# Performance work log

Hardware: AMD Instinct MI355X
Metric: run time of the kernel (lower is better)

Reference implementation:

```python
import jax, jax.numpy as jnp
import numpy as np

TOPK = 13
NUM_CLASSES = 80
ALPHA = 1.0
BETA = 6.0
EPS = 1e-9


def _ciou(gt, pd, eps=1e-7):
    """CIoU between gt (B,M,1,4) and pd (B,1,N,4) xyxy boxes -> (B,M,N)."""
    g_x1, g_y1, g_x2, g_y2 = (gt[..., i] for i in range(4))
    p_x1, p_y1, p_x2, p_y2 = (pd[..., i] for i in range(4))
    iw = jnp.clip(jnp.minimum(g_x2, p_x2) - jnp.maximum(g_x1, p_x1), 0.0)
    ih = jnp.clip(jnp.minimum(g_y2, p_y2) - jnp.maximum(g_y1, p_y1), 0.0)
    inter = iw * ih
    w1, h1 = g_x2 - g_x1, g_y2 - g_y1 + eps
    w2, h2 = p_x2 - p_x1, p_y2 - p_y1 + eps
    union = w1 * h1 + w2 * h2 - inter + eps
    iou = inter / union
    cw = jnp.maximum(g_x2, p_x2) - jnp.minimum(g_x1, p_x1)  # enclosing box
    ch = jnp.maximum(g_y2, p_y2) - jnp.minimum(g_y1, p_y1)
    c2 = cw * cw + ch * ch + eps
    rho2 = ((p_x1 + p_x2 - g_x1 - g_x2) ** 2 + (p_y1 + p_y2 - g_y1 - g_y2) ** 2) / 4.0
    v = (4.0 / jnp.pi ** 2) * (jnp.arctan(w2 / h2) - jnp.arctan(w1 / h1)) ** 2
    a = jax.lax.stop_gradient(v / (v - iou + (1.0 + eps)))  # torch.no_grad alpha
    return iou - (rho2 / c2 + v * a)


def setup_inputs() -> dict:
    key = jax.random.key(0)
    ks = jax.random.split(key, 7)
    B, N, M, C = 16, 8400, 32, NUM_CLASSES
    pd_scores = jax.random.uniform(ks[0], (B, N, C), dtype=jnp.float32)
    # YOLO-style anchor centers for 640x640, strides 8/16/32 -> 8400 points
    pts = []
    for s in (8, 16, 32):
        g = 640 // s
        xs = (jnp.arange(g, dtype=jnp.float32) + 0.5) * s
        xx, yy = jnp.meshgrid(xs, xs, indexing="xy")
        pts.append(jnp.stack([xx.ravel(), yy.ravel()], axis=-1))
    anc_points = jnp.concatenate(pts, axis=0)  # (8400, 2)
    ctr = anc_points[None] + jax.random.normal(ks[1], (B, N, 2)) * 8.0
    wh = jax.random.uniform(ks[2], (B, N, 2), minval=8.0, maxval=128.0)
    pd_bboxes = jnp.concatenate([ctr - wh / 2, ctr + wh / 2], axis=-1)
    gctr = jax.random.uniform(ks[3], (B, M, 2), minval=32.0, maxval=608.0)
    gwh = jax.random.uniform(ks[4], (B, M, 2), minval=16.0, maxval=256.0)
    gt_bboxes = jnp.concatenate([gctr - gwh / 2, gctr + gwh / 2], axis=-1)
    gt_labels = jax.random.randint(ks[5], (B, M, 1), 0, C)
    counts = jax.random.randint(ks[6], (B, 1), 1, M + 1)
    mask_gt = (jnp.arange(M)[None, :] < counts)[..., None]  # (B, M, 1) bool prefix-valid
    return {"pd_scores": pd_scores, "pd_bboxes": pd_bboxes, "anc_points": anc_points,
            "gt_labels": gt_labels, "gt_bboxes": gt_bboxes, "mask_gt": mask_gt}


def reference(pd_scores, pd_bboxes, anc_points, gt_labels, gt_bboxes, mask_gt):
    B, N, C = pd_scores.shape
    M = gt_bboxes.shape[1]
    mask_gt2 = mask_gt[..., 0]  # (B, M) bool
    # --- anchors whose centers lie inside each GT box ---
    lt = gt_bboxes[:, :, None, :2]  # (B, M, 1, 2)
    rb = gt_bboxes[:, :, None, 2:]
    anc = anc_points[None, None]    # (1, 1, N, 2)
    deltas = jnp.concatenate([anc - lt, rb - anc], axis=-1)  # (B, M, N, 4)
    mask_in_gts = jnp.min(deltas, axis=-1) > 1e-9            # (B, M, N)
    valid = mask_in_gts & mask_gt2[:, :, None]
    # --- alignment metric = score^alpha * ciou^beta (masked) ---
    cls = gt_labels[..., 0]                      # (B, M)
    scores_t = jnp.swapaxes(pd_scores, 1, 2)     # (B, C, N)
    bbox_scores = jnp.where(valid, scores_t[jnp.arange(B)[:, None], cls], 0.0)  # (B, M, N)
    overlaps = jnp.where(valid, jnp.clip(_ciou(gt_bboxes[:, :, None], pd_bboxes[:, None]), 0.0), 0.0)
    align_metric = bbox_scores ** ALPHA * overlaps ** BETA
    # --- top-k candidate anchors per GT ---
    _, topk_idx = jax.lax.top_k(align_metric, TOPK)          # (B, M, TOPK)
    bi = jnp.arange(B)[:, None, None]
    mi = jnp.arange(M)[None, :, None]
    src = jnp.broadcast_to(mask_gt2[:, :, None], topk_idx.shape)
    mask_topk = jnp.zeros((B, M, N), dtype=bool).at[bi, mi, topk_idx].set(src)
    mask_pos = mask_topk & valid                             # (B, M, N)
    # --- resolve anchors claimed by multiple GTs: keep highest CIoU ---
    fg_count = jnp.sum(mask_pos, axis=1)                     # (B, N)
    best_gt = jnp.argmax(overlaps, axis=1)                   # (B, N)
    is_max = jnp.arange(M)[None, :, None] == best_gt[:, None, :]
    mask_pos_f = jnp.where(fg_count[:, None, :] > 1, is_max, mask_pos).astype(pd_scores.dtype)
    fg_mask = jnp.sum(mask_pos_f, axis=1)                    # (B, N) float 0/1
    target_gt_idx = jnp.argmax(mask_pos_f, axis=1)           # (B, N)
    # --- gather targets ---
    brow = jnp.arange(B)[:, None]
    target_labels = cls[brow, target_gt_idx]                 # (B, N)
    target_bboxes = gt_bboxes[brow, target_gt_idx]           # (B, N, 4)
    target_scores = jax.nn.one_hot(target_labels, C, dtype=jnp.float32) * fg_mask[..., None]
    # --- normalize scores by per-GT best metric/overlap ---
    align_metric = align_metric * mask_pos_f
    pos_align = jnp.max(align_metric, axis=-1, keepdims=True)            # (B, M, 1)
    pos_over = jnp.max(overlaps * mask_pos_f, axis=-1, keepdims=True)    # (B, M, 1)
    norm_align = jnp.max(align_metric * pos_over / (pos_align + EPS), axis=1)  # (B, N)
    target_scores = target_scores * norm_align[..., None]
    return target_labels, target_bboxes, target_scores, fg_mask > 0, target_gt_idx
```

## Files before the change

### kernel.cpp

```cpp
#include <hip/hip_runtime.h>
#include <math.h>

#define B_ 16
#define N_ 8400
#define M_ 32
#define C_ 80
#define TOPK_ 13
#define KL_ 16

__device__ __forceinline__ bool in_gt(double ax, double ay,
    double gx1, double gy1, double gx2, double gy2) {
  return (ax - gx1 > 1e-9) && (ay - gy1 > 1e-9) &&
         (gx2 - ax > 1e-9) && (gy2 - ay > 1e-9);
}

__device__ __forceinline__ double ciou_ov(
    double px1, double py1, double px2, double py2,
    double gx1, double gy1, double gx2, double gy2,
    double atp, double atg) {
  double iw = fmin(gx2, px2) - fmax(gx1, px1); iw = iw > 0.0 ? iw : 0.0;
  double ih = fmin(gy2, py2) - fmax(gy1, py1); ih = ih > 0.0 ? ih : 0.0;
  double inter = iw * ih;
  double w1 = gx2 - gx1, h1 = gy2 - gy1 + 1e-7;
  double w2 = px2 - px1, h2 = py2 - py1 + 1e-7;
  double uni = w1 * h1 + w2 * h2 - inter + 1e-7;
  double iou = inter / uni;
  double cw = fmax(gx2, px2) - fmin(gx1, px1);
  double ch = fmax(gy2, py2) - fmin(gy1, py1);
  double c2 = cw * cw + ch * ch + 1e-7;
  double dx = px1 + px2 - gx1 - gx2, dy = py1 + py2 - gy1 - gy2;
  double rho2 = (dx * dx + dy * dy) * 0.25;
  double dv = atp - atg;
  double v = (4.0 / (M_PI * M_PI)) * dv * dv;
  double a = v / (v - iou + (1.0 + 1e-7));
  double c = iou - (rho2 / c2 + v * a);
  return c > 0.0 ? c : 0.0;
}

#define MERGE_LISTS(av, ai, bv, bi)                                          \
  {                                                                          \
    _Pragma("unroll")                                                        \
    for (int j = 0; j < KL_; ++j) {                                          \
      double vb = bv[KL_ - 1 - j]; int ib = bi[KL_ - 1 - j];                 \
      bool take = (vb > av[j]) || (vb == av[j] && ib < ai[j]);               \
      av[j] = take ? vb : av[j];                                             \
      ai[j] = take ? ib : ai[j];                                             \
    }                                                                        \
    _Pragma("unroll")                                                        \
    for (int dd = 8; dd >= 1; dd >>= 1) {                                    \
      _Pragma("unroll")                                                      \
      for (int j = 0; j < KL_; ++j) {                                        \
        if (!(j & dd)) {                                                     \
          int kk = j | dd;                                                   \
          bool sw = (av[kk] > av[j]) ||                                      \
                    (av[kk] == av[j] && ai[kk] < ai[j]);                     \
          double xv = av[j]; int xi = ai[j];                                 \
          av[j] = sw ? av[kk] : av[j]; ai[j] = sw ? ai[kk] : ai[j];          \
          av[kk] = sw ? xv : av[kk];   ai[kk] = sw ? xi : ai[kk];            \
        }                                                                    \
      }                                                                      \
    }                                                                        \
  }

__global__ __launch_bounds__(256) void k_prep(
    const float* __restrict__ pd_bboxes, const float* __restrict__ gt_bboxes,
    const unsigned char* __restrict__ raw,
    double* __restrict__ atp, double* __restrict__ atg,
    unsigned char* __restrict__ mask) {
  int gid = blockIdx.x * 256 + threadIdx.x;
  if (gid < B_ * N_) {
    double x1 = pd_bboxes[(size_t)gid * 4 + 0], y1 = pd_bboxes[(size_t)gid * 4 + 1];
    double x2 = pd_bboxes[(size_t)gid * 4 + 2], y2 = pd_bboxes[(size_t)gid * 4 + 3];
    atp[gid] = atan((x2 - x1) / (y2 - y1 + 1e-7));
  }
  if (gid < B_ * M_) {
    double x1 = gt_bboxes[gid * 4 + 0], y1 = gt_bboxes[gid * 4 + 1];
    double x2 = gt_bboxes[gid * 4 + 2], y2 = gt_bboxes[gid * 4 + 3];
    atg[gid] = atan((x2 - x1) / (y2 - y1 + 1e-7));
  }
  if (blockIdx.x == 0) {
    __shared__ int s_bad;
    int t = threadIdx.x;
    if (t == 0) s_bad = 0;
    __syncthreads();
    if (t < B_) {
      int cnt = 0; bool seen0 = false; bool bad = false;
      for (int m = 0; m < M_; ++m) {
        unsigned char v = raw[t * M_ + m];
        if (v > 1) { bad = true; break; }
        if (v) { if (seen0) { bad = true; break; } ++cnt; }
        else seen0 = true;
      }
      if (cnt < 1) bad = true;
      if (bad) atomicOr(&s_bad, 1);
    }
    __syncthreads();
    bool ok = (s_bad == 0);
    const int* ri = (const int*)raw;
    for (int i = t; i < B_ * M_; i += 256)
      mask[i] = ok ? (raw[i] ? 1 : 0) : ((ri[i] != 0) ? 1 : 0);
  }
}

__global__ __launch_bounds__(256) void k_topk(
    const float* __restrict__ pd_scores, const float* __restrict__ pd_bboxes,
    const float* __restrict__ anc, const int* __restrict__ gt_labels,
    const float* __restrict__ gt_bboxes, const unsigned char* __restrict__ mask,
    const double* __restrict__ atp, const double* __restrict__ atg,
    unsigned int* __restrict__ MPB) {
  int row = blockIdx.x;
  if (!mask[row]) return;
  int b = row >> 5, m = row & 31;
  int t = threadIdx.x;

  double gx1 = gt_bboxes[row * 4 + 0], gy1 = gt_bboxes[row * 4 + 1];
  double gx2 = gt_bboxes[row * 4 + 2], gy2 = gt_bboxes[row * 4 + 3];
  double atgm = atg[row];
  int cls = gt_labels[row];

  const float4* pb4 = (const float4*)(pd_bboxes + (size_t)b * N_ * 4);
  const float2* an2 = (const float2*)anc;
  const double* ap  = atp + (size_t)b * N_;
  const float*  scp = pd_scores + (size_t)b * N_ * C_ + cls;

  double tv[KL_]; int ti[KL_];
#pragma unroll
  for (int j = 0; j < KL_; ++j) { tv[j] = -1.0; ti[j] = 0x7fffffff; }

  auto body = [&](int n) {
    float2 a2 = an2[n];
    bool val = in_gt((double)a2.x, (double)a2.y, gx1, gy1, gx2, gy2);
    double am = 0.0;
    if (val) {
      float4 pbox = pb4[n];
      double ov = ciou_ov((double)pbox.x, (double)pbox.y, (double)pbox.z,
                          (double)pbox.w, gx1, gy1, gx2, gy2, ap[n], atgm);
      double o2 = ov * ov;
      am = (double)scp[(size_t)n * C_] * (o2 * o2 * o2);
    }
    if (am > tv[TOPK_ - 1]) {
      double cv = am; int ci = n;
#pragma unroll
      for (int j = 0; j < TOPK_; ++j) {
        bool sw = (cv > tv[j]) || (cv == tv[j] && ci < ti[j]);
        double xv = tv[j]; int xi = ti[j];
        if (sw) { tv[j] = cv; ti[j] = ci; cv = xv; ci = xi; }
      }
    }
  };

  for (int it = 0; it < 32; ++it) body(t + it * 256);
  if (t < N_ - 8192) body(t + 8192);

#pragma unroll
  for (int d = 1; d <= 32; d <<= 1) {
    double bv[KL_]; int bi[KL_];
#pragma unroll
    for (int j = 0; j < KL_; ++j) {
      bv[j] = __shfl_xor(tv[j], d, 64);
      bi[j] = __shfl_xor(ti[j], d, 64);
    }
    MERGE_LISTS(tv, ti, bv, bi)
  }

  __shared__ double s_v[4 * KL_];
  __shared__ int    s_i[4 * KL_];
  __shared__ int    s_sel[TOPK_];
  int wave = t >> 6, lane = t & 63;
  if (lane == 0) {
#pragma unroll
    for (int j = 0; j < KL_; ++j) { s_v[wave * KL_ + j] = tv[j]; s_i[wave * KL_ + j] = ti[j]; }
  }
  __syncthreads();
  if (t == 0) {
    double av[KL_]; int ai[KL_];
#pragma unroll
    for (int j = 0; j < KL_; ++j) { av[j] = s_v[j]; ai[j] = s_i[j]; }
    for (int w = 1; w < 4; ++w) {
      double bv[KL_]; int bi[KL_];
#pragma unroll
      for (int j = 0; j < KL_; ++j) { bv[j] = s_v[w * KL_ + j]; bi[j] = s_i[w * KL_ + j]; }
      MERGE_LISTS(av, ai, bv, bi)
    }
#pragma unroll
    for (int j = 0; j < TOPK_; ++j) s_sel[j] = ai[j];
  }
  __syncthreads();

  if (t < TOPK_) {
    int n = s_sel[t];
    float2 a2 = an2[n];
    if (in_gt((double)a2.x, (double)a2.y, gx1, gy1, gx2, gy2))
      atomicOr(&MPB[(size_t)b * N_ + n], 1u << m);
  }
}

__global__ __launch_bounds__(256) void k_colassign(
    const float* __restrict__ pd_scores, const float* __restrict__ pd_bboxes,
    const float* __restrict__ anc, const int* __restrict__ gt_labels,
    const float* __restrict__ gt_bboxes, const unsigned char* __restrict__ mask,
    const double* __restrict__ atp, const double* __restrict__ atg,
    const unsigned int* __restrict__ MPB,
    unsigned char* __restrict__ TG, unsigned char* __restrict__ FG,
    float* __restrict__ AMC,
    unsigned int* __restrict__ PAL, unsigned int* __restrict__ POV) {
  int b = blockIdx.y;
  int n = blockIdx.x * 256 + threadIdx.x;

  __shared__ float s_g[M_][4];
  __shared__ double s_atg[M_];
  __shared__ int s_cls[M_];
  __shared__ unsigned char s_msk[M_];
  if (threadIdx.x < M_) {
    int gi = b * M_ + threadIdx.x;
    s_g[threadIdx.x][0] = gt_bboxes[gi * 4 + 0];
    s_g[threadIdx.x][1] = gt_bboxes[gi * 4 + 1];
    s_g[threadIdx.x][2] = gt_bboxes[gi * 4 + 2];
    s_g[threadIdx.x][3] = gt_bboxes[gi * 4 + 3];
    s_atg[threadIdx.x] = atg[gi];
    s_cls[threadIdx.x] = gt_labels[gi];
    s_msk[threadIdx.x] = mask[gi];
  }
  __syncthreads();
  if (n >= N_) return;

  size_t i = (size_t)b * N_ + n;
  unsigned int mpb = MPB[i];
  int cnt = __popc(mpb);
  int tg = 0; unsigned char fg = 0;
  double ov = 0.0;

  if (cnt >= 1) {
    fg = 1;
    float2 a2 = ((const float2*)anc)[n];
    float4 pbox = ((const float4*)(pd_bboxes + (size_t)b * N_ * 4))[n];
    double atpn = atp[i];
    if (cnt == 1) {
      tg = __ffs(mpb) - 1;
      double g0 = s_g[tg][0], g1 = s_g[tg][1], g2 = s_g[tg][2], g3 = s_g[tg][3];
      bool val = s_msk[tg] && in_gt((double)a2.x, (double)a2.y, g0, g1, g2, g3);
      ov = val ? ciou_ov((double)pbox.x, (double)pbox.y, (double)pbox.z,
                         (double)pbox.w, g0, g1, g2, g3, atpn, s_atg[tg]) : 0.0;
    } else {
      double best = -1.0;
      for (int mm = 0; mm < M_; ++mm) {
        double g0 = s_g[mm][0], g1 = s_g[mm][1], g2 = s_g[mm][2], g3 = s_g[mm][3];
        bool val = s_msk[mm] && in_gt((double)a2.x, (double)a2.y, g0, g1, g2, g3);
        double o = val ? ciou_ov((double)pbox.x, (double)pbox.y, (double)pbox.z,
                                 (double)pbox.w, g0, g1, g2, g3, atpn, s_atg[mm])
                       : 0.0;
        if (o > best) { best = o; tg = mm; }
      }
      ov = best;
    }
  }

  TG[i] = (unsigned char)tg;
  FG[i] = fg;

  if (fg) {
    double o2 = ov * ov;
    double am = (double)pd_scores[i * C_ + s_cls[tg]] * (o2 * o2 * o2);
    float ovf = (float)ov, amf = (float)am;
    AMC[i] = amf;
    atomicMax(&PAL[b * M_ + tg], __float_as_uint(amf));
    atomicMax(&POV[b * M_ + tg], __float_as_uint(ovf));
  }
}

__global__ __launch_bounds__(256) void k_emit(
    const int* __restrict__ gt_labels, const float* __restrict__ gt_bboxes,
    const unsigned char* __restrict__ TG, const unsigned char* __restrict__ FG,
    const float* __restrict__ AMC,
    const unsigned int* __restrict__ PAL, const unsigned int* __restrict__ POV,
    float* __restrict__ out) {
  int b = blockIdx.y;
  int n0 = blockIdx.x * 64;
  int t = threadIdx.x;

  __shared__ float s_g[M_][4];
  __shared__ int s_cls[M_];
  __shared__ float s_pal[M_], s_pov[M_];
  __shared__ float s_na[64];
  __shared__ int   s_lab[64];
  __shared__ int   s_tg[64];
  __shared__ unsigned char s_fg[64];
  if (t < M_) {
    int gi = b * M_ + t;
    s_g[t][0] = gt_bboxes[gi * 4 + 0];
    s_g[t][1] = gt_bboxes[gi * 4 + 1];
    s_g[t][2] = gt_bboxes[gi * 4 + 2];
    s_g[t][3] = gt_bboxes[gi * 4 + 3];
    s_cls[t] = gt_labels[gi];
    s_pal[t] = __uint_as_float(PAL[gi]);
    s_pov[t] = __uint_as_float(POV[gi]);
  }
  __syncthreads();

  if (t < 64) {
    int n = n0 + t;
    if (n < N_) {
      size_t i = (size_t)b * N_ + n;
      int tg = TG[i];
      unsigned char fg = FG[i];
      float na = 0.0f;
      if (fg) {
        double am = (double)AMC[i];
        na = (float)(am * (double)s_pov[tg] / ((double)s_pal[tg] + 1e-9));
      }
      s_na[t] = na; s_lab[t] = s_cls[tg]; s_tg[t] = tg; s_fg[t] = fg;
    }
  }
  __syncthreads();

  float* o0 = out;
  float* o1 = out + (size_t)B_ * N_;
  float* o2 = out + (size_t)B_ * N_ * 5;
  float* o3 = out + (size_t)B_ * N_ * 85;
  float* o4 = out + (size_t)B_ * N_ * 86;

  if (t < 64) {
    int n = n0 + t;
    if (n < N_) {
      size_t i = (size_t)b * N_ + n;
      o0[i] = (float)s_lab[t];
      o3[i] = s_fg[t] ? 1.0f : 0.0f;
      o4[i] = (float)s_tg[t];
      int tg = s_tg[t];
      ((float4*)o1)[i] = make_float4(s_g[tg][0], s_g[tg][1], s_g[tg][2], s_g[tg][3]);
    }
  }

#pragma unroll
  for (int k = 0; k < 5; ++k) {
    int id = t + k * 256;
    int a = id / 20, j = id % 20;
    int n = n0 + a;
    if (n < N_) {
      int lab = s_lab[a];
      float na = s_fg[a] ? s_na[a] : 0.0f;
      int c0 = 4 * j;
      float4 w;
      w.x = (c0 + 0 == lab) ? na : 0.0f;
      w.y = (c0 + 1 == lab) ? na : 0.0f;
      w.z = (c0 + 2 == lab) ? na : 0.0f;
      w.w = (c0 + 3 == lab) ? na : 0.0f;
      ((float4*)(o2 + ((size_t)b * N_ + n) * C_))[j] = w;
    }
  }
}

extern "C" void kernel_launch(void* const* d_in, const int* in_sizes, int n_in,
                              void* d_out, int out_size, void* d_ws, size_t ws_size,
                              hipStream_t stream) {
  const float* pd_scores = (const float*)d_in[0];
  const float* pd_bboxes = (const float*)d_in[1];
  const float* anc       = (const float*)d_in[2];
  const int*   gt_labels = (const int*)d_in[3];
  const float* gt_bboxes = (const float*)d_in[4];
  const unsigned char* mask_raw = (const unsigned char*)d_in[5];

  char* ws = (char*)d_ws;
  size_t off = 0;
  double* ATP = (double*)(ws + off); off += (size_t)B_ * N_ * 8;
  double* ATG = (double*)(ws + off); off += (size_t)B_ * M_ * 8;
  unsigned int* MPB = (unsigned int*)(ws + off); size_t z0 = off; off += (size_t)B_ * N_ * 4;
  unsigned int* PAL = (unsigned int*)(ws + off); off += (size_t)B_ * M_ * 4;
  unsigned int* POV = (unsigned int*)(ws + off); off += (size_t)B_ * M_ * 4;
  size_t zlen = off - z0;
  unsigned char* TG   = (unsigned char*)(ws + off); off += (size_t)B_ * N_;
  unsigned char* FG   = (unsigned char*)(ws + off); off += (size_t)B_ * N_;
  float* AMC = (float*)(ws + off); off += (size_t)B_ * N_ * 4;
  unsigned char* MASK = (unsigned char*)(ws + off); off += (size_t)B_ * M_;

  hipMemsetAsync(ws + z0, 0, zlen, stream);

  k_prep<<<(B_ * N_ + 255) / 256, 256, 0, stream>>>(pd_bboxes, gt_bboxes,
                                                    mask_raw, ATP, ATG, MASK);
  k_topk<<<B_ * M_, 256, 0, stream>>>(pd_scores, pd_bboxes, anc, gt_labels,
                                      gt_bboxes, MASK, ATP, ATG, MPB);
  dim3 gbn((N_ + 255) / 256, B_);
  k_colassign<<<gbn, 256, 0, stream>>>(pd_scores, pd_bboxes, anc, gt_labels,
                                       gt_bboxes, MASK, ATP, ATG, MPB,
                                       TG, FG, AMC, PAL, POV);
  dim3 gem((N_ + 63) / 64, B_);
  k_emit<<<gem, 256, 0, stream>>>(gt_labels, gt_bboxes, TG, FG, AMC, PAL, POV,
                                  (float*)d_out);
}
```

Before: 176.1 us.

## Pre-gather per-GT class scores into a contiguous buffer before top-k

Adds a kernel that streams pd_scores coalesced through shared memory and writes, for each (batch, gt) row, the score of that GT's class at every anchor into a contiguous SG buffer. k_topk and k_colassign then read SG with unit stride instead of doing strided 320-byte-apart loads from pd_scores. This trades one full coalesced pass over pd_scores (~43MB) plus a 17MB write for removing uncoalesced gathers, and adds a kernel launch and extra workspace.

```diff
diff --git a/kernel.cpp b/kernel.cpp
--- a/kernel.cpp
+++ b/kernel.cpp
@@ -7,6 +7,7 @@
 #define C_ 80
 #define TOPK_ 13
 #define KL_ 16
+#define GT_ 128
 
 __device__ __forceinline__ bool in_gt(double ax, double ay,
     double gx1, double gy1, double gx2, double gy2) {
@@ -102,9 +103,41 @@
   }
 }
 
+__global__ __launch_bounds__(256) void k_gath(
+    const float* __restrict__ pd_scores, const int* __restrict__ gt_labels,
+    float* __restrict__ SG) {
+  int b = blockIdx.y;
+  int n0 = blockIdx.x * GT_;
+  int t = threadIdx.x;
+  int nn = min(GT_, N_ - n0);
+
+  __shared__ float s_sc[GT_ * C_];
+  __shared__ int s_cls[M_];
+  if (t < M_) s_cls[t] = gt_labels[b * M_ + t];
+
+  const float4* src = (const float4*)(pd_scores + ((size_t)b * N_ + n0) * C_);
+  float4* dst = (float4*)s_sc;
+  int tot4 = nn * (C_ / 4);
+#pragma unroll
+  for (int k = 0; k < GT_ * (C_ / 4) / 256; ++k) {
+    int id = t + k * 256;
+    if (id < tot4) dst[id] = src[id];
+  }
+  __syncthreads();
+
+  int nl = t & (GT_ - 1);
+  int mh = t >> 7;
+#pragma unroll
+  for (int mm = 0; mm < M_ / 2; ++mm) {
+    int m = mm * 2 + mh;
+    if (nl < nn)
+      SG[(size_t)(b * M_ + m) * N_ + n0 + nl] = s_sc[nl * C_ + s_cls[m]];
+  }
+}
+
 __global__ __launch_bounds__(256) void k_topk(
-    const float* __restrict__ pd_scores, const float* __restrict__ pd_bboxes,
-    const float* __restrict__ anc, const int* __restrict__ gt_labels,
+    const float* __restrict__ SG, const float* __restrict__ pd_bboxes,
+    const float* __restrict__ anc,
     const float* __restrict__ gt_bboxes, const unsigned char* __restrict__ mask,
     const double* __restrict__ atp, const double* __restrict__ atg,
     unsigned int* __restrict__ MPB) {
@@ -116,12 +149,11 @@
   double gx1 = gt_bboxes[row * 4 + 0], gy1 = gt_bboxes[row * 4 + 1];
   double gx2 = gt_bboxes[row * 4 + 2], gy2 = gt_bboxes[row * 4 + 3];
   double atgm = atg[row];
-  int cls = gt_labels[row];
 
   const float4* pb4 = (const float4*)(pd_bboxes + (size_t)b * N_ * 4);
   const float2* an2 = (const float2*)anc;
   const double* ap  = atp + (size_t)b * N_;
-  const float*  scp = pd_scores + (size_t)b * N_ * C_ + cls;
+  const float*  sg  = SG + (size_t)row * N_;
 
   double tv[KL_]; int ti[KL_];
 #pragma unroll
@@ -136,7 +168,7 @@
       double ov = ciou_ov((double)pbox.x, (double)pbox.y, (double)pbox.z,
                           (double)pbox.w, gx1, gy1, gx2, gy2, ap[n], atgm);
       double o2 = ov * ov;
-      am = (double)scp[(size_t)n * C_] * (o2 * o2 * o2);
+      am = (double)sg[n] * (o2 * o2 * o2);
     }
     if (am > tv[TOPK_ - 1]) {
       double cv = am; int ci = n;
@@ -196,8 +228,8 @@
 }
 
 __global__ __launch_bounds__(256) void k_colassign(
-    const float* __restrict__ pd_scores, const float* __restrict__ pd_bboxes,
-    const float* __restrict__ anc, const int* __restrict__ gt_labels,
+    const float* __restrict__ SG, const float* __restrict__ pd_bboxes,
+    const float* __restrict__ anc,
     const float* __restrict__ gt_bboxes, const unsigned char* __restrict__ mask,
     const double* __restrict__ atp, const double* __restrict__ atg,
     const unsigned int* __restrict__ MPB,
@@ -209,7 +241,6 @@
 
   __shared__ float s_g[M_][4];
   __shared__ double s_atg[M_];
-  __shared__ int s_cls[M_];
   __shared__ unsigned char s_msk[M_];
   if (threadIdx.x < M_) {
     int gi = b * M_ + threadIdx.x;
@@ -218,7 +249,6 @@
     s_g[threadIdx.x][2] = gt_bboxes[gi * 4 + 2];
     s_g[threadIdx.x][3] = gt_bboxes[gi * 4 + 3];
     s_atg[threadIdx.x] = atg[gi];
-    s_cls[threadIdx.x] = gt_labels[gi];
     s_msk[threadIdx.x] = mask[gi];
   }
   __syncthreads();
@@ -260,7 +290,7 @@
 
   if (fg) {
     double o2 = ov * ov;
-    double am = (double)pd_scores[i * C_ + s_cls[tg]] * (o2 * o2 * o2);
+    double am = (double)SG[(size_t)(b * M_ + tg) * N_ + n] * (o2 * o2 * o2);
     float ovf = (float)ov, amf = (float)am;
     AMC[i] = amf;
     atomicMax(&PAL[b * M_ + tg], __float_as_uint(amf));
@@ -364,6 +394,7 @@
   size_t off = 0;
   double* ATP = (double*)(ws + off); off += (size_t)B_ * N_ * 8;
   double* ATG = (double*)(ws + off); off += (size_t)B_ * M_ * 8;
+  float*  SG  = (float*)(ws + off);  off += (size_t)B_ * M_ * N_ * 4;
   unsigned int* MPB = (unsigned int*)(ws + off); size_t z0 = off; off += (size_t)B_ * N_ * 4;
   unsigned int* PAL = (unsigned int*)(ws + off); off += (size_t)B_ * M_ * 4;
   unsigned int* POV = (unsigned int*)(ws + off); off += (size_t)B_ * M_ * 4;
@@ -377,10 +408,12 @@
 
   k_prep<<<(B_ * N_ + 255) / 256, 256, 0, stream>>>(pd_bboxes, gt_bboxes,
                                                     mask_raw, ATP, ATG, MASK);
-  k_topk<<<B_ * M_, 256, 0, stream>>>(pd_scores, pd_bboxes, anc, gt_labels,
+  dim3 gg((N_ + GT_ - 1) / GT_, B_);
+  k_gath<<<gg, 256, 0, stream>>>(pd_scores, gt_labels, SG);
+  k_topk<<<B_ * M_, 256, 0, stream>>>(SG, pd_bboxes, anc,
                                       gt_bboxes, MASK, ATP, ATG, MPB);
   dim3 gbn((N_ + 255) / 256, B_);
-  k_colassign<<<gbn, 256, 0, stream>>>(pd_scores, pd_bboxes, anc, gt_labels,
+  k_colassign<<<gbn, 256, 0, stream>>>(SG, pd_bboxes, anc,
                                        gt_bboxes, MASK, ATP, ATG, MPB,
                                        TG, FG, AMC, PAL, POV);
   dim3 gem((N_ + 63) / 64, B_);
```

New measurement: 189.7 us. 7.7% more time.

## Compact in-box candidates per GT before top-k and wave-parallelize multi-GT ties

Applied to the files above, without the earlier changes.

Replaces the per-GT full scan of all 8400 anchors with a candidate-compaction kernel that computes CIoU and align metric only for anchors inside each GT box and appends them atomically to per-row buffers. A row-select kernel then does top-k over those compacted candidates and pads with zero-metric anchors in index order to keep the reference tie-breaking. Anchor atan is computed inline instead of being precomputed into a buffer, and the memset is folded into the prep kernel. Anchors with multiple positive GTs now cooperate across a wavefront, one GT per lane, for the argmax over overlaps. The cost is atomic contention, a fixed per-row capacity (MAXC) that could silently drop candidates, and a larger workspace.

```diff
diff --git a/kernel.cpp b/kernel.cpp
--- a/kernel.cpp
+++ b/kernel.cpp
@@ -7,6 +7,9 @@
 #define C_ 80
 #define TOPK_ 13
 #define KL_ 16
+#define MAXC_ 2048
+#define MZ_ 4
+#define MG_ (M_ / MZ_)
 
 __device__ __forceinline__ bool in_gt(double ax, double ay,
     double gx1, double gy1, double gx2, double gy2) {
@@ -62,21 +65,18 @@
     }                                                                        \
   }
 
-__global__ __launch_bounds__(256) void k_prep(
-    const float* __restrict__ pd_bboxes, const float* __restrict__ gt_bboxes,
-    const unsigned char* __restrict__ raw,
-    double* __restrict__ atp, double* __restrict__ atg,
-    unsigned char* __restrict__ mask) {
+__global__ __launch_bounds__(256) void k_prep0(
+    const float* __restrict__ gt_bboxes, const unsigned char* __restrict__ raw,
+    double* __restrict__ atg, unsigned char* __restrict__ mask,
+    unsigned int* __restrict__ MPB, unsigned int* __restrict__ CNT,
+    unsigned int* __restrict__ PAL, unsigned int* __restrict__ POV) {
   int gid = blockIdx.x * 256 + threadIdx.x;
-  if (gid < B_ * N_) {
-    double x1 = pd_bboxes[(size_t)gid * 4 + 0], y1 = pd_bboxes[(size_t)gid * 4 + 1];
-    double x2 = pd_bboxes[(size_t)gid * 4 + 2], y2 = pd_bboxes[(size_t)gid * 4 + 3];
-    atp[gid] = atan((x2 - x1) / (y2 - y1 + 1e-7));
-  }
+  if (gid < B_ * N_) MPB[gid] = 0u;
   if (gid < B_ * M_) {
     double x1 = gt_bboxes[gid * 4 + 0], y1 = gt_bboxes[gid * 4 + 1];
     double x2 = gt_bboxes[gid * 4 + 2], y2 = gt_bboxes[gid * 4 + 3];
     atg[gid] = atan((x2 - x1) / (y2 - y1 + 1e-7));
+    CNT[gid] = 0u; PAL[gid] = 0u; POV[gid] = 0u;
   }
   if (blockIdx.x == 0) {
     __shared__ int s_bad;
@@ -102,55 +102,98 @@
   }
 }
 
-__global__ __launch_bounds__(256) void k_topk(
+__global__ __launch_bounds__(256) void k_cand(
     const float* __restrict__ pd_scores, const float* __restrict__ pd_bboxes,
     const float* __restrict__ anc, const int* __restrict__ gt_labels,
     const float* __restrict__ gt_bboxes, const unsigned char* __restrict__ mask,
-    const double* __restrict__ atp, const double* __restrict__ atg,
-    unsigned int* __restrict__ MPB) {
+    const double* __restrict__ atg,
+    unsigned int* __restrict__ CNT, double* __restrict__ CV,
+    int* __restrict__ CI) {
+  int b = blockIdx.y, t = threadIdx.x;
+  int m0 = blockIdx.z * MG_;
+  int n = blockIdx.x * 256 + t;
+
+  __shared__ double s_g[MG_][4];
+  __shared__ double s_atg[MG_];
+  __shared__ int s_cls[MG_];
+  __shared__ unsigned char s_msk[MG_];
+  __shared__ int s_any;
+  if (t == 0) s_any = 0;
+  __syncthreads();
+  if (t < MG_) {
+    int row = b * M_ + m0 + t;
+    unsigned char mk = mask[row];
+    s_msk[t] = mk;
+    if (mk) atomicOr(&s_any, 1);
+    s_g[t][0] = (double)gt_bboxes[row * 4 + 0];
+    s_g[t][1] = (double)gt_bboxes[row * 4 + 1];
+    s_g[t][2] = (double)gt_bboxes[row * 4 + 2];
+    s_g[t][3] = (double)gt_bboxes[row * 4 + 3];
+    s_atg[t] = atg[row];
+    s_cls[t] = gt_labels[row];
+  }
+  __syncthreads();
+  if (!s_any) return;
+  if (n >= N_) return;
+
+  float2 a2 = ((const float2*)anc)[n];
+  double ax = (double)a2.x, ay = (double)a2.y;
+  bool have = false;
+  double px1 = 0, py1 = 0, px2 = 0, py2 = 0, atpn = 0;
+  const float* srow = pd_scores + ((size_t)b * N_ + n) * C_;
+
+  for (int mm = 0; mm < MG_; ++mm) {
+    if (!s_msk[mm]) continue;
+    double gx1 = s_g[mm][0], gy1 = s_g[mm][1], gx2 = s_g[mm][2], gy2 = s_g[mm][3];
+    if (!in_gt(ax, ay, gx1, gy1, gx2, gy2)) continue;
+    if (!have) {
+      float4 pb = ((const float4*)(pd_bboxes + (size_t)b * N_ * 4))[n];
+      px1 = (double)pb.x; py1 = (double)pb.y;
+      px2 = (double)pb.z; py2 = (double)pb.w;
+      atpn = atan((px2 - px1) / ((py2 - py1) + 1e-7));
+      have = true;
+    }
+    double ov = ciou_ov(px1, py1, px2, py2, gx1, gy1, gx2, gy2, atpn, s_atg[mm]);
+    double o2 = ov * ov;
+    double am = (double)srow[s_cls[mm]] * (o2 * o2 * o2);
+    int row = b * M_ + m0 + mm;
+    unsigned int idx = atomicAdd(&CNT[row], 1u);
+    if (idx < MAXC_) {
+      CV[(size_t)row * MAXC_ + idx] = am;
+      CI[(size_t)row * MAXC_ + idx] = n;
+    }
+  }
+}
+
+__global__ __launch_bounds__(256) void k_rowsel(
+    const double* __restrict__ CV, const int* __restrict__ CI,
+    const unsigned int* __restrict__ CNT,
+    const float* __restrict__ anc, const float* __restrict__ gt_bboxes,
+    const unsigned char* __restrict__ mask, unsigned int* __restrict__ MPB) {
   int row = blockIdx.x;
   if (!mask[row]) return;
   int b = row >> 5, m = row & 31;
   int t = threadIdx.x;
-
-  double gx1 = gt_bboxes[row * 4 + 0], gy1 = gt_bboxes[row * 4 + 1];
-  double gx2 = gt_bboxes[row * 4 + 2], gy2 = gt_bboxes[row * 4 + 3];
-  double atgm = atg[row];
-  int cls = gt_labels[row];
-
-  const float4* pb4 = (const float4*)(pd_bboxes + (size_t)b * N_ * 4);
-  const float2* an2 = (const float2*)anc;
-  const double* ap  = atp + (size_t)b * N_;
-  const float*  scp = pd_scores + (size_t)b * N_ * C_ + cls;
+  int cnt = (int)CNT[row]; if (cnt > MAXC_) cnt = MAXC_;
+  const double* cv = CV + (size_t)row * MAXC_;
+  const int*    ci = CI + (size_t)row * MAXC_;
 
   double tv[KL_]; int ti[KL_];
 #pragma unroll
   for (int j = 0; j < KL_; ++j) { tv[j] = -1.0; ti[j] = 0x7fffffff; }
 
-  auto body = [&](int n) {
-    float2 a2 = an2[n];
-    bool val = in_gt((double)a2.x, (double)a2.y, gx1, gy1, gx2, gy2);
-    double am = 0.0;
-    if (val) {
-      float4 pbox = pb4[n];
-      double ov = ciou_ov((double)pbox.x, (double)pbox.y, (double)pbox.z,
-                          (double)pbox.w, gx1, gy1, gx2, gy2, ap[n], atgm);
-      double o2 = ov * ov;
-      am = (double)scp[(size_t)n * C_] * (o2 * o2 * o2);
-    }
-    if (am > tv[TOPK_ - 1]) {
-      double cv = am; int ci = n;
+  for (int i = t; i < cnt; i += 256) {
+    double v = cv[i]; int idx = ci[i];
+    if (v > tv[TOPK_ - 1] || (v == tv[TOPK_ - 1] && idx < ti[TOPK_ - 1])) {
+      double cvv = v; int cii = idx;
 #pragma unroll
       for (int j = 0; j < TOPK_; ++j) {
-        bool sw = (cv > tv[j]) || (cv == tv[j] && ci < ti[j]);
+        bool sw = (cvv > tv[j]) || (cvv == tv[j] && cii < ti[j]);
         double xv = tv[j]; int xi = ti[j];
-        if (sw) { tv[j] = cv; ti[j] = ci; cv = xv; ci = xi; }
+        if (sw) { tv[j] = cvv; ti[j] = cii; cvv = xv; cii = xi; }
       }
     }
-  };
-
-  for (int it = 0; it < 32; ++it) body(t + it * 256);
-  if (t < N_ - 8192) body(t + 8192);
+  }
 
 #pragma unroll
   for (int d = 1; d <= 32; d <<= 1) {
@@ -166,6 +209,7 @@
   __shared__ double s_v[4 * KL_];
   __shared__ int    s_i[4 * KL_];
   __shared__ int    s_sel[TOPK_];
+  __shared__ int    s_p;
   int wave = t >> 6, lane = t & 63;
   if (lane == 0) {
 #pragma unroll
@@ -182,16 +226,33 @@
       for (int j = 0; j < KL_; ++j) { bv[j] = s_v[w * KL_ + j]; bi[j] = s_i[w * KL_ + j]; }
       MERGE_LISTS(av, ai, bv, bi)
     }
-#pragma unroll
-    for (int j = 0; j < TOPK_; ++j) s_sel[j] = ai[j];
+    int p = 0;
+#pragma unroll
+    for (int j = 0; j < TOPK_; ++j)
+      if (av[j] > 0.0) s_sel[p++] = ai[j];
+    int nn = 0, slot = p;
+    while (slot < TOPK_) {
+      bool ispos = false;
+      for (int q = 0; q < p; ++q) ispos |= (s_sel[q] == nn);
+      if (!ispos) s_sel[slot++] = nn | 0x40000000;
+      ++nn;
+    }
+    s_p = p;
   }
   __syncthreads();
 
   if (t < TOPK_) {
-    int n = s_sel[t];
-    float2 a2 = an2[n];
-    if (in_gt((double)a2.x, (double)a2.y, gx1, gy1, gx2, gy2))
-      atomicOr(&MPB[(size_t)b * N_ + n], 1u << m);
+    int e = s_sel[t];
+    if (t < s_p) {
+      atomicOr(&MPB[(size_t)b * N_ + e], 1u << m);
+    } else {
+      int n = e & 0x3fffffff;
+      double gx1 = gt_bboxes[row * 4 + 0], gy1 = gt_bboxes[row * 4 + 1];
+      double gx2 = gt_bboxes[row * 4 + 2], gy2 = gt_bboxes[row * 4 + 3];
+      float2 a2 = ((const float2*)anc)[n];
+      if (in_gt((double)a2.x, (double)a2.y, gx1, gy1, gx2, gy2))
+        atomicOr(&MPB[(size_t)b * N_ + n], 1u << m);
+    }
   }
 }
 
@@ -199,65 +260,81 @@
     const float* __restrict__ pd_scores, const float* __restrict__ pd_bboxes,
     const float* __restrict__ anc, const int* __restrict__ gt_labels,
     const float* __restrict__ gt_bboxes, const unsigned char* __restrict__ mask,
-    const double* __restrict__ atp, const double* __restrict__ atg,
-    const unsigned int* __restrict__ MPB,
+    const double* __restrict__ atg, const unsigned int* __restrict__ MPB,
     unsigned char* __restrict__ TG, unsigned char* __restrict__ FG,
     float* __restrict__ AMC,
     unsigned int* __restrict__ PAL, unsigned int* __restrict__ POV) {
   int b = blockIdx.y;
-  int n = blockIdx.x * 256 + threadIdx.x;
-
-  __shared__ float s_g[M_][4];
+  int t = threadIdx.x;
+  int n = blockIdx.x * 256 + t;
+  int lane = t & 63;
+  bool act = (n < N_);
+
+  __shared__ double s_g[M_][4];
   __shared__ double s_atg[M_];
   __shared__ int s_cls[M_];
   __shared__ unsigned char s_msk[M_];
-  if (threadIdx.x < M_) {
-    int gi = b * M_ + threadIdx.x;
-    s_g[threadIdx.x][0] = gt_bboxes[gi * 4 + 0];
-    s_g[threadIdx.x][1] = gt_bboxes[gi * 4 + 1];
-    s_g[threadIdx.x][2] = gt_bboxes[gi * 4 + 2];
-    s_g[threadIdx.x][3] = gt_bboxes[gi * 4 + 3];
-    s_atg[threadIdx.x] = atg[gi];
-    s_cls[threadIdx.x] = gt_labels[gi];
-    s_msk[threadIdx.x] = mask[gi];
-  }
-  __syncthreads();
-  if (n >= N_) return;
-
-  size_t i = (size_t)b * N_ + n;
-  unsigned int mpb = MPB[i];
+  if (t < M_) {
+    int gi = b * M_ + t;
+    s_g[t][0] = (double)gt_bboxes[gi * 4 + 0];
+    s_g[t][1] = (double)gt_bboxes[gi * 4 + 1];
+    s_g[t][2] = (double)gt_bboxes[gi * 4 + 2];
+    s_g[t][3] = (double)gt_bboxes[gi * 4 + 3];
+    s_atg[t] = atg[gi];
+    s_cls[t] = gt_labels[gi];
+    s_msk[t] = mask[gi];
+  }
+  __syncthreads();
+
+  size_t i = (size_t)b * N_ + (act ? n : 0);
+  unsigned int mpb = act ? MPB[i] : 0u;
   int cnt = __popc(mpb);
-  int tg = 0; unsigned char fg = 0;
-  double ov = 0.0;
-
-  if (cnt >= 1) {
+
+  double ax = 0, ay = 0, px1 = 0, py1 = 0, px2 = 0, py2 = 0;
+  if (act && cnt >= 1) {
+    float2 a2 = ((const float2*)anc)[n];
+    float4 pb = ((const float4*)(pd_bboxes + (size_t)b * N_ * 4))[n];
+    ax = (double)a2.x; ay = (double)a2.y;
+    px1 = (double)pb.x; py1 = (double)pb.y; px2 = (double)pb.z; py2 = (double)pb.w;
+  }
+
+  int tg = 0; unsigned char fg = 0; double ov = 0.0;
+
+  if (act && cnt == 1) {
     fg = 1;
-    float2 a2 = ((const float2*)anc)[n];
-    float4 pbox = ((const float4*)(pd_bboxes + (size_t)b * N_ * 4))[n];
-    double atpn = atp[i];
-    if (cnt == 1) {
-      tg = __ffs(mpb) - 1;
-      double g0 = s_g[tg][0], g1 = s_g[tg][1], g2 = s_g[tg][2], g3 = s_g[tg][3];
-      bool val = s_msk[tg] && in_gt((double)a2.x, (double)a2.y, g0, g1, g2, g3);
-      ov = val ? ciou_ov((double)pbox.x, (double)pbox.y, (double)pbox.z,
-                         (double)pbox.w, g0, g1, g2, g3, atpn, s_atg[tg]) : 0.0;
-    } else {
-      double best = -1.0;
-      for (int mm = 0; mm < M_; ++mm) {
-        double g0 = s_g[mm][0], g1 = s_g[mm][1], g2 = s_g[mm][2], g3 = s_g[mm][3];
-        bool val = s_msk[mm] && in_gt((double)a2.x, (double)a2.y, g0, g1, g2, g3);
-        double o = val ? ciou_ov((double)pbox.x, (double)pbox.y, (double)pbox.z,
-                                 (double)pbox.w, g0, g1, g2, g3, atpn, s_atg[mm])
-                       : 0.0;
-        if (o > best) { best = o; tg = mm; }
-      }
-      ov = best;
-    }
-  }
+    tg = __ffs(mpb) - 1;
+    double atpn = atan((px2 - px1) / ((py2 - py1) + 1e-7));
+    double g0 = s_g[tg][0], g1 = s_g[tg][1], g2 = s_g[tg][2], g3 = s_g[tg][3];
+    bool val = s_msk[tg] && in_gt(ax, ay, g0, g1, g2, g3);
+    ov = val ? ciou_ov(px1, py1, px2, py2, g0, g1, g2, g3, atpn, s_atg[tg]) : 0.0;
+  }
+
+  unsigned long long flagged = __ballot(act && cnt > 1);
+  while (flagged) {
+    int src = __ffsll(flagged) - 1;
+    flagged &= flagged - 1;
+    double qx  = __shfl(ax, src, 64),  qy  = __shfl(ay, src, 64);
+    double q1  = __shfl(px1, src, 64), q2  = __shfl(py1, src, 64);
+    double q3  = __shfl(px2, src, 64), q4  = __shfl(py2, src, 64);
+    double atq = atan((q3 - q1) / ((q4 - q2) + 1e-7));
+    int mm = lane & 31;
+    double g0 = s_g[mm][0], g1 = s_g[mm][1], g2 = s_g[mm][2], g3 = s_g[mm][3];
+    bool val = s_msk[mm] && in_gt(qx, qy, g0, g1, g2, g3);
+    double o = val ? ciou_ov(q1, q2, q3, q4, g0, g1, g2, g3, atq, s_atg[mm]) : 0.0;
+    int cm = mm;
+#pragma unroll
+    for (int d = 1; d < 32; d <<= 1) {
+      double oo = __shfl_xor(o, d, 64);
+      int    om = __shfl_xor(cm, d, 64);
+      if (oo > o || (oo == o && om < cm)) { o = oo; cm = om; }
+    }
+    if (lane == src) { fg = 1; tg = cm; ov = o; }
+  }
+
+  if (!act) return;
 
   TG[i] = (unsigned char)tg;
   FG[i] = fg;
-
   if (fg) {
     double o2 = ov * ov;
     double am = (double)pd_scores[i * C_ + s_cls[tg]] * (o2 * o2 * o2);
@@ -362,26 +439,27 @@
 
   char* ws = (char*)d_ws;
   size_t off = 0;
-  double* ATP = (double*)(ws + off); off += (size_t)B_ * N_ * 8;
+  double* CV  = (double*)(ws + off); off += (size_t)B_ * M_ * MAXC_ * 8;
   double* ATG = (double*)(ws + off); off += (size_t)B_ * M_ * 8;
-  unsigned int* MPB = (unsigned int*)(ws + off); size_t z0 = off; off += (size_t)B_ * N_ * 4;
+  int*    CI  = (int*)(ws + off);    off += (size_t)B_ * M_ * MAXC_ * 4;
+  unsigned int* MPB = (unsigned int*)(ws + off); off += (size_t)B_ * N_ * 4;
+  unsigned int* CNT = (unsigned int*)(ws + off); off += (size_t)B_ * M_ * 4;
   unsigned int* PAL = (unsigned int*)(ws + off); off += (size_t)B_ * M_ * 4;
   unsigned int* POV = (unsigned int*)(ws + off); off += (size_t)B_ * M_ * 4;
-  size_t zlen = off - z0;
   unsigned char* TG   = (unsigned char*)(ws + off); off += (size_t)B_ * N_;
   unsigned char* FG   = (unsigned char*)(ws + off); off += (size_t)B_ * N_;
   float* AMC = (float*)(ws + off); off += (size_t)B_ * N_ * 4;
   unsigned char* MASK = (unsigned char*)(ws + off); off += (size_t)B_ * M_;
 
-  hipMemsetAsync(ws + z0, 0, zlen, stream);
-
-  k_prep<<<(B_ * N_ + 255) / 256, 256, 0, stream>>>(pd_bboxes, gt_bboxes,
-                                                    mask_raw, ATP, ATG, MASK);
-  k_topk<<<B_ * M_, 256, 0, stream>>>(pd_scores, pd_bboxes, anc, gt_labels,
-                                      gt_bboxes, MASK, ATP, ATG, MPB);
+  k_prep0<<<(B_ * N_ + 255) / 256, 256, 0, stream>>>(gt_bboxes, mask_raw, ATG,
+                                                     MASK, MPB, CNT, PAL, POV);
+  dim3 gc((N_ + 255) / 256, B_, MZ_);
+  k_cand<<<gc, 256, 0, stream>>>(pd_scores, pd_bboxes, anc, gt_labels,
+                                 gt_bboxes, MASK, ATG, CNT, CV, CI);
+  k_rowsel<<<B_ * M_, 256, 0, stream>>>(CV, CI, CNT, anc, gt_bboxes, MASK, MPB);
   dim3 gbn((N_ + 255) / 256, B_);
   k_colassign<<<gbn, 256, 0, stream>>>(pd_scores, pd_bboxes, anc, gt_labels,
-                                       gt_bboxes, MASK, ATP, ATG, MPB,
+                                       gt_bboxes, MASK, ATG, MPB,
                                        TG, FG, AMC, PAL, POV);
   dim3 gem((N_ + 63) / 64, B_);
   k_emit<<<gem, 256, 0, stream>>>(gt_labels, gt_bboxes, TG, FG, AMC, PAL, POV,
```

Result: faster. 162.5 us (-7.7%).
